# Performance work log

Measured on AMD Instinct MI355X. Metric: run time of the kernel, lower is better.

Reference implementation:

```python
import jax, jax.numpy as jnp
from jax import lax
import numpy as np

NDIM = 256
BATCH = 65536
NROT = NDIM * (NDIM - 1) // 2  # comb(ndim, 2) = 32640


def _givens_mat(rots, ii, jj, ndim):
    """Product G_last @ ... @ G_1 of Givens rotations in combinations order.

    Left-multiplying by G(i, j, theta) only modifies rows i and j, so we apply
    each rotation as a rank-2 row update instead of a full matmul (same math
    as the original `plane_rot_mat @ mat` loop).
    """
    def step(mat, carry):
        i, j, th = carry
        c = jnp.cos(th)
        s = jnp.sin(th)
        ri = mat[i]
        rj = mat[j]
        mat = mat.at[i].set(c * ri - s * rj)
        mat = mat.at[j].set(s * ri + c * rj)
        return mat, None

    mat0 = jnp.eye(ndim, dtype=jnp.complex64)
    mat, _ = lax.scan(step, mat0, (ii, jj, rots))
    return mat


def setup_inputs() -> dict:
    key = jax.random.key(0)
    k1, k2, k3, k4 = jax.random.split(key, 4)
    x = jax.random.normal(k1, (BATCH, NDIM), dtype=jnp.float32)
    rots1 = 0.1 * jax.random.normal(k2, (NROT,), dtype=jnp.float32)
    phases = 0.1 * jax.random.normal(k3, (NDIM,), dtype=jnp.float32)
    rots2 = 0.1 * jax.random.normal(k4, (NROT,), dtype=jnp.float32)
    return {"x": x, "rots1": rots1, "phases": phases, "rots2": rots2}


def reference(x, rots1, phases, rots2):
    ndim = x.shape[1]
    # np.triu_indices(ndim, 1) enumerates (i, j) pairs in the same row-major
    # order as itertools.combinations(range(ndim), 2).
    ii_np, jj_np = np.triu_indices(ndim, k=1)
    ii = jnp.asarray(ii_np, dtype=jnp.int32)
    jj = jnp.asarray(jj_np, dtype=jnp.int32)

    # vector_norm: row-wise L2 normalization
    xn = x / jnp.linalg.norm(x, axis=1, keepdims=True)
    xc = xn.astype(jnp.complex64)

    # rot1: y = x @ M1.T with M1 = G_last @ ... @ G_1
    M1 = _givens_mat(rots1, ii, jj, ndim)
    y = xc @ M1.T

    # phase_transforms: x @ diag(exp(i*phases)) == elementwise phase multiply
    y = y * jnp.exp(1j * phases)

    # rot2
    M2 = _givens_mat(rots2, ii, jj, ndim)
    y = y @ M2.T

    # measure: |.|^2
    return jnp.abs(y) ** 2
```

## Files before the change

kernel.cpp:

```cpp
#include <hip/hip_runtime.h>
#include <stdint.h>
#include <math.h>

#define NDIM 256
#define BATCH 65536
#define NROT 32640

typedef float  f32x4 __attribute__((ext_vector_type(4)));
typedef short  s16x8 __attribute__((ext_vector_type(8)));
typedef unsigned int u32x4 __attribute__((ext_vector_type(4)));
typedef unsigned int u32x2 __attribute__((ext_vector_type(2)));

static __device__ __forceinline__ unsigned short f2bf(float f) {
    unsigned int u = __float_as_uint(f);
    u += 0x7fffu + ((u >> 16) & 1u);
    return (unsigned short)(u >> 16);
}
static __device__ __forceinline__ float bf2f(unsigned short h) {
    return __uint_as_float(((unsigned)h) << 16);
}

static __device__ __forceinline__ void split4(f32x4 v, u32x2* hi, u32x2* lo) {
    unsigned short h[4], l[4];
    #pragma unroll
    for (int i = 0; i < 4; i++) {
        h[i] = f2bf(v[i]);
        l[i] = f2bf(v[i] - bf2f(h[i]));
    }
    *hi = (u32x2){ (unsigned)h[0] | ((unsigned)h[1] << 16),
                   (unsigned)h[2] | ((unsigned)h[3] << 16) };
    *lo = (u32x2){ (unsigned)l[0] | ((unsigned)l[1] << 16),
                   (unsigned)l[2] | ((unsigned)l[3] << 16) };
}
static __device__ __forceinline__ void split8(const float* v, u32x4* hi, u32x4* lo) {
    unsigned short h[8], l[8];
    #pragma unroll
    for (int i = 0; i < 8; i++) {
        h[i] = f2bf(v[i]);
        l[i] = f2bf(v[i] - bf2f(h[i]));
    }
    *hi = (u32x4){ (unsigned)h[0] | ((unsigned)h[1] << 16),
                   (unsigned)h[2] | ((unsigned)h[3] << 16),
                   (unsigned)h[4] | ((unsigned)h[5] << 16),
                   (unsigned)h[6] | ((unsigned)h[7] << 16) };
    *lo = (u32x4){ (unsigned)l[0] | ((unsigned)l[1] << 16),
                   (unsigned)l[2] | ((unsigned)l[3] << 16),
                   (unsigned)l[4] | ((unsigned)l[5] << 16),
                   (unsigned)l[6] | ((unsigned)l[7] << 16) };
}

static __device__ __forceinline__ int sweep_bound(int k, int pblk) {
    int target = k * (NROT / pblk);
    int best = 0, bd = 0x7fffffff;
    for (int i = 0; i <= 256; i += 4) {
        int pre = i * 255 - (i * (i - 1)) / 2;
        int d = pre - target; d = (d < 0) ? -d : d;
        if (d < bd) { bd = d; best = i; }
    }
    return best;
}

__global__ __launch_bounds__(64) void k_blocks(const float* __restrict__ r1,
                                               const float* __restrict__ r2,
                                               float* __restrict__ bmats, int pblk,
                                               const float* __restrict__ xg,
                                               unsigned short* __restrict__ xbf) {
    __shared__ float colb[264 * 64];
    __shared__ float2 csb[256 * 4];
    __shared__ float2 tri[24 * 6];
    const int nblk = 8 * pblk;

    if ((int)blockIdx.x >= nblk) {
        const int lane = threadIdx.x;
        const int r0 = ((int)blockIdx.x - nblk) * 16;
        #pragma unroll
        for (int hb = 0; hb < 2; hb++) {
            f32x4 v[8];
            #pragma unroll
            for (int i = 0; i < 8; i++)
                v[i] = *(const f32x4*)&xg[(size_t)(r0 + hb * 8 + i) * 256 + lane * 4];
            #pragma unroll
            for (int i = 0; i < 8; i++) {
                float s = v[i][0] * v[i][0] + v[i][1] * v[i][1]
                        + v[i][2] * v[i][2] + v[i][3] * v[i][3];
                #pragma unroll
                for (int off = 32; off; off >>= 1) s += __shfl_xor(s, off, 64);
                float sc = 1.0f / sqrtf(s);
                unsigned short h0 = f2bf(v[i][0] * sc), h1 = f2bf(v[i][1] * sc);
                unsigned short h2 = f2bf(v[i][2] * sc), h3 = f2bf(v[i][3] * sc);
                u32x2 pk = { (unsigned)h0 | ((unsigned)h1 << 16),
                             (unsigned)h2 | ((unsigned)h3 << 16) };
                *(u32x2*)&xbf[(size_t)(r0 + hb * 8 + i) * 256 + lane * 4] = pk;
            }
        }
        return;
    }

    const int t = threadIdx.x;
    const int bid = blockIdx.x;
    const int chunk = bid & 3;
    const int b = (bid >> 2) % pblk;
    const int set = (bid >> 2) / pblk;
    const int col0 = chunk * 64;
    const float* rots = set ? r2 : r1;

    const int s0 = sweep_bound(b, pblk);
    const int s1 = sweep_bound(b + 1, pblk);
    const int ngroups = (s1 - s0) >> 2;

    {
        const f32x4 z = {0.f, 0.f, 0.f, 0.f};
        #pragma unroll 11
        for (int q = 0; q < 66; q++)
            *(f32x4*)&colb[(q * 64 + t) * 4] = z;
        colb[(col0 + t) * 64 + t] = 1.0f;
    }

    for (int k = t; k < ngroups * 6; k += 64) {
        int g = k / 6, q = k - g * 6;
        int a  = (q < 3) ? 0 : ((q < 5) ? 1 : 2);
        int bb = (q < 3) ? (q + 1) : ((q < 5) ? (q - 1) : 3);
        int m0 = s0 + g * 4;
        int m = m0 + a;
        int base = m * 255 - (m * (m - 1)) / 2;
        float th = rots[base - m - 1 + (m0 + bb)];
        float sv, cv; sincosf(th, &sv, &cv);
        tri[k] = make_float2(cv, sv);
    }

    for (int g = 0; g < ngroups; g++) {
        const int m0 = s0 + g * 4;
        int off[4];
        #pragma unroll
        for (int a = 0; a < 4; a++) {
            int m = m0 + a;
            int base = m * 255 - (m * (m - 1)) / 2;
            off[a] = base - m - 1;
        }
        const int n_j = 252 - m0;
        const int n_p = (n_j > 0) ? ((n_j + 7) & ~7) : 0;

        for (int k = t; k < n_p * 4; k += 64) {
            int jj = k >> 2, a = k & 3;
            int j = m0 + 4 + jj;
            if (j < 256) {
                float th = rots[off[a] + j];
                float sv, cv; sincosf(th, &sv, &cv);
                csb[k] = make_float2(cv, sv);
            } else {
                csb[k] = make_float2(1.f, 0.f);
            }
        }

        float u0 = colb[(m0 + 0) * 64 + t];
        float u1 = colb[(m0 + 1) * 64 + t];
        float u2 = colb[(m0 + 2) * 64 + t];
        float u3 = colb[(m0 + 3) * 64 + t];

        {
            float2 cv; float nr;
            cv = tri[g * 6 + 0]; nr = cv.y * u0 + cv.x * u1; u0 = cv.x * u0 - cv.y * u1; u1 = nr;
            cv = tri[g * 6 + 1]; nr = cv.y * u0 + cv.x * u2; u0 = cv.x * u0 - cv.y * u2; u2 = nr;
            cv = tri[g * 6 + 2]; nr = cv.y * u0 + cv.x * u3; u0 = cv.x * u0 - cv.y * u3; u3 = nr;
            cv = tri[g * 6 + 3]; nr = cv.y * u1 + cv.x * u2; u1 = cv.x * u1 - cv.y * u2; u2 = nr;
            cv = tri[g * 6 + 4]; nr = cv.y * u1 + cv.x * u3; u1 = cv.x * u1 - cv.y * u3; u3 = nr;
            cv = tri[g * 6 + 5]; nr = cv.y * u2 + cv.x * u3; u2 = cv.x * u2 - cv.y * u3; u3 = nr;
        }

        if (n_p > 0) {
            float rbuf[8];
            #pragma unroll
            for (int p = 0; p < 8; p++)
                rbuf[p] = colb[(m0 + 4 + p) * 64 + t];
            for (int c = 0; c < n_p; c += 8) {
                #pragma unroll
                for (int p = 0; p < 8; p++) {
                    const int j = m0 + 4 + c + p;
                    float r = rbuf[p];
                    int jn = j + 8; jn = (jn < 263) ? jn : 263;
                    rbuf[p] = colb[jn * 64 + t];
                    float2 a0 = csb[(c + p) * 4 + 0];
                    float2 a1 = csb[(c + p) * 4 + 1];
                    float2 a2 = csb[(c + p) * 4 + 2];
                    float2 a3 = csb[(c + p) * 4 + 3];
                    float nr;
                    nr = a0.y * u0 + a0.x * r; u0 = a0.x * u0 - a0.y * r; r = nr;
                    nr = a1.y * u1 + a1.x * r; u1 = a1.x * u1 - a1.y * r; r = nr;
                    nr = a2.y * u2 + a2.x * r; u2 = a2.x * u2 - a2.y * r; r = nr;
                    nr = a3.y * u3 + a3.x * r; u3 = a3.x * u3 - a3.y * r; r = nr;
                    colb[j * 64 + t] = r;
                }
            }
        }
        colb[(m0 + 0) * 64 + t] = u0;
        colb[(m0 + 1) * 64 + t] = u1;
        colb[(m0 + 2) * 64 + t] = u2;
        colb[(m0 + 3) * 64 + t] = u3;
    }

    float* outm = bmats + (size_t)(set * pblk + b) * 65536;
    for (int r = 0; r < 256; r++)
        outm[(size_t)r * 256 + col0 + t] = colb[r * 64 + t];
}

__global__ __launch_bounds__(256) void k_combine(const float* __restrict__ src,
                                                 float* __restrict__ dst,
                                                 int half, int pblk) {
    const int by = blockIdx.y;
    const int set = by / half, pidx = by % half;
    const int stride = pblk / (2 * half);
    const int s0A = sweep_bound((2 * pidx + 1) * stride, pblk);
    const float* Am = src + (size_t)(set * 2 * half + 2 * pidx + 1) * 65536;
    const float* Bm = src + (size_t)(set * 2 * half + 2 * pidx) * 65536;
    float* Dm = dst + (size_t)(set * half + pidx) * 65536;
    const int tr = blockIdx.x >> 2, tc = blockIdx.x & 3;
    const int tid = threadIdx.x;

    if (tr * 64 + 64 <= s0A) {
        #pragma unroll
        for (int it = 0; it < 4; it++) {
            int flat = tid + it * 256;
            int r = flat >> 4, c4 = flat & 15;
            size_t idx = (size_t)(tr * 64 + r) * 256 + tc * 64 + c4 * 4;
            *(f32x4*)&Dm[idx] = *(const f32x4*)&Bm[idx];
        }
        return;
    }
    const int kb0 = (tr * 64 >= s0A) ? (s0A >> 5) : 0;

    __shared__ unsigned short Ahi[64 * 40], Alo[64 * 40];
    __shared__ unsigned short Bhi[64 * 40], Blo[64 * 40];

    const int lane = tid & 63, w = tid >> 6;
    const int mh = (w >> 1) * 32, nh = (w & 1) * 32;
    const int l15 = lane & 15, lq = lane >> 4;
    const int bn = tid & 63, bkq = tid >> 6;

    f32x4 acc[2][2];
    #pragma unroll
    for (int i = 0; i < 2; i++)
        #pragma unroll
        for (int j = 0; j < 2; j++) acc[i][j] = (f32x4){0.f, 0.f, 0.f, 0.f};

    for (int kb = kb0; kb < 8; kb++) {
        __syncthreads();
        #pragma unroll
        for (int it = 0; it < 2; it++) {
            int flat = tid + it * 256;
            int r = flat >> 3, c4 = flat & 7;
            f32x4 v = *(const f32x4*)&Am[(size_t)(tr * 64 + r) * 256 + kb * 32 + c4 * 4];
            u32x2 hi, lo; split4(v, &hi, &lo);
            *(u32x2*)&Ahi[r * 40 + c4 * 4] = hi;
            *(u32x2*)&Alo[r * 40 + c4 * 4] = lo;
        }
        {
            float bv[8];
            #pragma unroll
            for (int i = 0; i < 8; i++)
                bv[i] = Bm[(size_t)(kb * 32 + bkq * 8 + i) * 256 + tc * 64 + bn];
            u32x4 hi, lo; split8(bv, &hi, &lo);
            *(u32x4*)&Bhi[bn * 40 + bkq * 8] = hi;
            *(u32x4*)&Blo[bn * 40 + bkq * 8] = lo;
        }
        __syncthreads();
        s16x8 ah[2], al[2], bh[2], bl[2];
        #pragma unroll
        for (int tm = 0; tm < 2; tm++) {
            ah[tm] = *(const s16x8*)&Ahi[(mh + tm * 16 + l15) * 40 + lq * 8];
            al[tm] = *(const s16x8*)&Alo[(mh + tm * 16 + l15) * 40 + lq * 8];
        }
        #pragma unroll
        for (int tn = 0; tn < 2; tn++) {
            bh[tn] = *(const s16x8*)&Bhi[(nh + tn * 16 + l15) * 40 + lq * 8];
            bl[tn] = *(const s16x8*)&Blo[(nh + tn * 16 + l15) * 40 + lq * 8];
        }
        #pragma unroll
        for (int tm = 0; tm < 2; tm++)
            #pragma unroll
            for (int tn = 0; tn < 2; tn++) {
                acc[tm][tn] = __builtin_amdgcn_mfma_f32_16x16x32_bf16(ah[tm], bh[tn], acc[tm][tn], 0, 0, 0);
                acc[tm][tn] = __builtin_amdgcn_mfma_f32_16x16x32_bf16(ah[tm], bl[tn], acc[tm][tn], 0, 0, 0);
                acc[tm][tn] = __builtin_amdgcn_mfma_f32_16x16x32_bf16(al[tm], bh[tn], acc[tm][tn], 0, 0, 0);
            }
    }
    #pragma unroll
    for (int tm = 0; tm < 2; tm++)
        #pragma unroll
        for (int tn = 0; tn < 2; tn++)
            #pragma unroll
            for (int r = 0; r < 4; r++)
                Dm[(size_t)(tr * 64 + mh + tm * 16 + lq * 4 + r) * 256
                   + tc * 64 + nh + tn * 16 + l15] = acc[tm][tn][r];
}

__global__ __launch_bounds__(256) void k_abt(const float* __restrict__ mats,
                                             const float* __restrict__ phases,
                                             unsigned short* __restrict__ abt) {
    const float* Am = mats + 65536;
    const float* Bm = mats;
    const int v = blockIdx.y;
    const int tr = blockIdx.x >> 2, tc = blockIdx.x & 3;
    const int tid = threadIdx.x;

    __shared__ unsigned short Ahi[64 * 40], Alo[64 * 40];
    __shared__ unsigned short Bhi[64 * 40], Blo[64 * 40];

    const int lane = tid & 63, w = tid >> 6;
    const int mh = (w >> 1) * 32, nh = (w & 1) * 32;
    const int l15 = lane & 15, lq = lane >> 4;
    const int bn = tid & 63, bkq = tid >> 6;

    f32x4 acc[2][2];
    #pragma unroll
    for (int i = 0; i < 2; i++)
        #pragma unroll
        for (int j = 0; j < 2; j++) acc[i][j] = (f32x4){0.f, 0.f, 0.f, 0.f};

    for (int kb = 0; kb < 8; kb++) {
        __syncthreads();
        #pragma unroll
        for (int it = 0; it < 2; it++) {
            int flat = tid + it * 256;
            int r = flat >> 3, c4 = flat & 7;
            f32x4 vv = *(const f32x4*)&Am[(size_t)(tr * 64 + r) * 256 + kb * 32 + c4 * 4];
            u32x2 hi, lo; split4(vv, &hi, &lo);
            *(u32x2*)&Ahi[r * 40 + c4 * 4] = hi;
            *(u32x2*)&Alo[r * 40 + c4 * 4] = lo;
        }
        {
            float bv[8];
            #pragma unroll
            for (int i = 0; i < 8; i++) {
                int kg = kb * 32 + bkq * 8 + i;
                float ph = phases[kg];
                float sc = v ? sinf(ph) : cosf(ph);
                bv[i] = Bm[(size_t)kg * 256 + tc * 64 + bn] * sc;
            }
            u32x4 hi, lo; split8(bv, &hi, &lo);
            *(u32x4*)&Bhi[bn * 40 + bkq * 8] = hi;
            *(u32x4*)&Blo[bn * 40 + bkq * 8] = lo;
        }
        __syncthreads();
        s16x8 ah[2], al[2], bh[2], bl[2];
        #pragma unroll
        for (int tm = 0; tm < 2; tm++) {
            ah[tm] = *(const s16x8*)&Ahi[(mh + tm * 16 + l15) * 40 + lq * 8];
            al[tm] = *(const s16x8*)&Alo[(mh + tm * 16 + l15) * 40 + lq * 8];
        }
        #pragma unroll
        for (int tn = 0; tn < 2; tn++) {
            bh[tn] = *(const s16x8*)&Bhi[(nh + tn * 16 + l15) * 40 + lq * 8];
            bl[tn] = *(const s16x8*)&Blo[(nh + tn * 16 + l15) * 40 + lq * 8];
        }
        #pragma unroll
        for (int tm = 0; tm < 2; tm++)
            #pragma unroll
            for (int tn = 0; tn < 2; tn++) {
                acc[tm][tn] = __builtin_amdgcn_mfma_f32_16x16x32_bf16(ah[tm], bh[tn], acc[tm][tn], 0, 0, 0);
                acc[tm][tn] = __builtin_amdgcn_mfma_f32_16x16x32_bf16(ah[tm], bl[tn], acc[tm][tn], 0, 0, 0);
                acc[tm][tn] = __builtin_amdgcn_mfma_f32_16x16x32_bf16(al[tm], bh[tn], acc[tm][tn], 0, 0, 0);
            }
    }
    #pragma unroll
    for (int tm = 0; tm < 2; tm++)
        #pragma unroll
        for (int tn = 0; tn < 2; tn++)
            #pragma unroll
            for (int r = 0; r < 4; r++)
                abt[(size_t)(v * 256 + tr * 64 + mh + tm * 16 + lq * 4 + r) * 256
                    + tc * 64 + nh + tn * 16 + l15] = f2bf(acc[tm][tn][r]);
}

__global__ __launch_bounds__(256) void k_norm(const float* __restrict__ x,
                                              float* __restrict__ invn) {
    const int row = blockIdx.x * 4 + (threadIdx.x >> 6);
    const int lane = threadIdx.x & 63;
    f32x4 v = *(const f32x4*)&x[(size_t)row * 256 + lane * 4];
    float s = v[0] * v[0] + v[1] * v[1] + v[2] * v[2] + v[3] * v[3];
    for (int off = 32; off; off >>= 1) s += __shfl_xor(s, off, 64);
    if (lane == 0) invn[row] = 1.0f / sqrtf(s);
}

#define BKP 136
__global__ __launch_bounds__(256) void k_gemm_bf(const unsigned short* __restrict__ xbf,
                                                 const unsigned short* __restrict__ abt,
                                                 float* __restrict__ out) {
    __shared__ unsigned short As[128 * BKP];
    __shared__ unsigned short Bs[128 * BKP];
    const int tid = threadIdx.x;
    const int cb = blockIdx.x;
    const int rb = blockIdx.y;
    const int lane = tid & 63, w = tid >> 6;

    f32x4 acc[16];
    #pragma unroll
    for (int i = 0; i < 16; i++) acc[i] = (f32x4){0.f, 0.f, 0.f, 0.f};

    int rA[8], cA[8], grB[8];
    #pragma unroll
    for (int it = 0; it < 8; it++) {
        int flat = tid + it * 256;
        rA[it] = flat >> 4; cA[it] = flat & 15;
        int r = rA[it];
        grB[it] = (r < 64) ? (cb * 64 + r) : (256 + cb * 64 + (r - 64));
    }

    u32x4 pa[8], pb[8];
    #pragma unroll
    for (int it = 0; it < 8; it++) {
        pa[it] = *(const u32x4*)&xbf[(size_t)(rb * 128 + rA[it]) * 256 + cA[it] * 8];
        pb[it] = *(const u32x4*)&abt[(size_t)grB[it] * 256 + cA[it] * 8];
    }
    #pragma unroll
    for (int it = 0; it < 8; it++) {
        *(u32x4*)&As[rA[it] * BKP + cA[it] * 8] = pa[it];
        *(u32x4*)&Bs[rA[it] * BKP + cA[it] * 8] = pb[it];
    }
    __syncthreads();
    #pragma unroll
    for (int it = 0; it < 8; it++) {
        pa[it] = *(const u32x4*)&xbf[(size_t)(rb * 128 + rA[it]) * 256 + 128 + cA[it] * 8];
        pb[it] = *(const u32x4*)&abt[(size_t)grB[it] * 256 + 128 + cA[it] * 8];
    }

    auto compute = [&]() {
        #pragma unroll
        for (int ks = 0; ks < 4; ks++) {
            const int k0 = ks * 32 + (lane >> 4) * 8;
            s16x8 a[2], b[8];
            #pragma unroll
            for (int tm = 0; tm < 2; tm++)
                a[tm] = *(const s16x8*)&As[(w * 32 + tm * 16 + (lane & 15)) * BKP + k0];
            #pragma unroll
            for (int tn = 0; tn < 8; tn++)
                b[tn] = *(const s16x8*)&Bs[(tn * 16 + (lane & 15)) * BKP + k0];
            #pragma unroll
            for (int tm = 0; tm < 2; tm++)
                #pragma unroll
                for (int tn = 0; tn < 8; tn++)
                    acc[tm * 8 + tn] = __builtin_amdgcn_mfma_f32_16x16x32_bf16(
                        a[tm], b[tn], acc[tm * 8 + tn], 0, 0, 0);
        }
    };
    compute();
    __syncthreads();
    #pragma unroll
    for (int it = 0; it < 8; it++) {
        *(u32x4*)&As[rA[it] * BKP + cA[it] * 8] = pa[it];
        *(u32x4*)&Bs[rA[it] * BKP + cA[it] * 8] = pb[it];
    }
    __syncthreads();
    compute();

    const int qr = lane >> 4, c = lane & 15;
    #pragma unroll
    for (int tm = 0; tm < 2; tm++) {
        #pragma unroll
        for (int tn = 0; tn < 4; tn++) {
            f32x4 p = acc[tm * 8 + tn];
            f32x4 q = acc[tm * 8 + tn + 4];
            #pragma unroll
            for (int r = 0; r < 4; r++) {
                int m = w * 32 + tm * 16 + qr * 4 + r;
                out[(size_t)(rb * 128 + m) * 256 + cb * 64 + tn * 16 + c] =
                    p[r] * p[r] + q[r] * q[r];
            }
        }
    }
}

__global__ __launch_bounds__(256) void k_gemm_f32(const float* __restrict__ x,
                                                  const unsigned short* __restrict__ abt,
                                                  const float* __restrict__ invn,
                                                  float* __restrict__ out) {
    __shared__ unsigned short As[128 * BKP];
    __shared__ unsigned short Bs[128 * BKP];
    const int tid = threadIdx.x;
    const int cb = blockIdx.x;
    const int rb = blockIdx.y;
    const int lane = tid & 63, w = tid >> 6;

    f32x4 acc[16];
    #pragma unroll
    for (int i = 0; i < 16; i++) acc[i] = (f32x4){0.f, 0.f, 0.f, 0.f};

    for (int kb = 0; kb < 2; kb++) {
        __syncthreads();
        #pragma unroll
        for (int it = 0; it < 16; it++) {
            int flat = tid + it * 256;
            int r = flat >> 5, c4 = flat & 31;
            f32x4 v = *(const f32x4*)&x[(size_t)(rb * 128 + r) * 256 + kb * 128 + c4 * 4];
            float sc = invn[rb * 128 + r];
            v[0] *= sc; v[1] *= sc; v[2] *= sc; v[3] *= sc;
            unsigned short h0 = f2bf(v[0]), h1 = f2bf(v[1]);
            unsigned short h2 = f2bf(v[2]), h3 = f2bf(v[3]);
            u32x2 pk = { (unsigned)h0 | ((unsigned)h1 << 16),
                         (unsigned)h2 | ((unsigned)h3 << 16) };
            *(u32x2*)&As[r * BKP + c4 * 4] = pk;
        }
        #pragma unroll
        for (int it = 0; it < 8; it++) {
            int flat = tid + it * 256;
            int r = flat >> 4, c8 = flat & 15;
            int gr = (r < 64) ? (cb * 64 + r) : (256 + cb * 64 + (r - 64));
            u32x4 vv = *(const u32x4*)&abt[(size_t)gr * 256 + kb * 128 + c8 * 8];
            *(u32x4*)&Bs[r * BKP + c8 * 8] = vv;
        }
        __syncthreads();
        #pragma unroll
        for (int ks = 0; ks < 4; ks++) {
            const int k0 = ks * 32 + (lane >> 4) * 8;
            s16x8 a[2], b[8];
            #pragma unroll
            for (int tm = 0; tm < 2; tm++)
                a[tm] = *(const s16x8*)&As[(w * 32 + tm * 16 + (lane & 15)) * BKP + k0];
            #pragma unroll
            for (int tn = 0; tn < 8; tn++)
                b[tn] = *(const s16x8*)&Bs[(tn * 16 + (lane & 15)) * BKP + k0];
            #pragma unroll
            for (int tm = 0; tm < 2; tm++)
                #pragma unroll
                for (int tn = 0; tn < 8; tn++)
                    acc[tm * 8 + tn] = __builtin_amdgcn_mfma_f32_16x16x32_bf16(
                        a[tm], b[tn], acc[tm * 8 + tn], 0, 0, 0);
        }
    }

    const int qr = lane >> 4, c = lane & 15;
    #pragma unroll
    for (int tm = 0; tm < 2; tm++) {
        #pragma unroll
        for (int tn = 0; tn < 4; tn++) {
            f32x4 p = acc[tm * 8 + tn];
            f32x4 q = acc[tm * 8 + tn + 4];
            #pragma unroll
            for (int r = 0; r < 4; r++) {
                int m = w * 32 + tm * 16 + qr * 4 + r;
                out[(size_t)(rb * 128 + m) * 256 + cb * 64 + tn * 16 + c] =
                    p[r] * p[r] + q[r] * q[r];
            }
        }
    }
}

extern "C" void kernel_launch(void* const* d_in, const int* in_sizes, int n_in,
                              void* d_out, int out_size, void* d_ws, size_t ws_size,
                              hipStream_t stream) {
    (void)in_sizes; (void)n_in; (void)out_size;
    const float* x      = (const float*)d_in[0];
    const float* rots1  = (const float*)d_in[1];
    const float* phases = (const float*)d_in[2];
    const float* rots2  = (const float*)d_in[3];
    float* out = (float*)d_out;
    char* ws = (char*)d_ws;

    const size_t MAT = 262144;
    int pblk = 32;
    while (pblk > 16 &&
           (size_t)3 * pblk * MAT + 2 * MAT + (size_t)BATCH * 512 > ws_size)
        pblk >>= 1;
    const size_t offA   = 0;
    const size_t offB   = offA + (size_t)2 * pblk * MAT;
    const size_t offABT = offB + (size_t)pblk * MAT;
    const size_t offINV = offABT + MAT;
    const size_t offXBF = offINV + MAT;
    const bool use_xbf = (offXBF + (size_t)BATCH * 512) <= ws_size;

    float*          A    = (float*)(ws + offA);
    float*          B    = (float*)(ws + offB);
    unsigned short* abt  = (unsigned short*)(ws + offABT);
    float*          invn = (float*)(ws + offINV);
    unsigned short* xbf  = (unsigned short*)(ws + offXBF);

    const int nblk = 8 * pblk;
    const int nxn  = use_xbf ? (BATCH / 16) : 0;
    k_blocks<<<nblk + nxn, 64, 0, stream>>>(rots1, rots2, A, pblk, x, xbf);

    float* srcp = A; float* dstp = B;
    for (int half = pblk / 2; half >= 1; half >>= 1) {
        k_combine<<<dim3(16, 2 * half), 256, 0, stream>>>(srcp, dstp, half, pblk);
        float* tmp = srcp; srcp = dstp; dstp = tmp;
    }
    k_abt<<<dim3(16, 2), 256, 0, stream>>>(srcp, phases, abt);

    if (use_xbf) {
        k_gemm_bf<<<dim3(4, BATCH / 128), 256, 0, stream>>>(xbf, abt, out);
    } else {
        k_norm<<<BATCH / 4, 256, 0, stream>>>(x, invn);
        k_gemm_f32<<<dim3(4, BATCH / 128), 256, 0, stream>>>(x, abt, invn, out);
    }
}
```

Measured before the change: 269.7 us.

## Precompute Givens sincos in a separate kernel and move normalization into first combine

Adds a small kernel that computes cos/sin for all rotations once into workspace, so k_blocks reads precomputed pairs instead of calling sincosf per element. The row normalization and bf16 conversion of x moves out of k_blocks and into extra blocks of the first k_combine launch, using one wave per row with 64 rows per block. The intent is to shorten the serial block-building phase and overlap the memory-bound normalization with combine work. It adds one kernel launch and reuses the B buffer as sincos scratch before combine overwrites it.

```diff
diff --git a/kernel.cpp b/kernel.cpp
--- a/kernel.cpp
+++ b/kernel.cpp
@@ -60,41 +60,20 @@
     return best;
 }
 
-__global__ __launch_bounds__(64) void k_blocks(const float* __restrict__ r1,
-                                               const float* __restrict__ r2,
-                                               float* __restrict__ bmats, int pblk,
-                                               const float* __restrict__ xg,
-                                               unsigned short* __restrict__ xbf) {
+__global__ __launch_bounds__(256) void k_cs(const float* __restrict__ r1,
+                                            const float* __restrict__ r2,
+                                            float2* __restrict__ cs) {
+    int i = blockIdx.x * 256 + threadIdx.x;
+    float th = (i < NROT) ? r1[i] : r2[i - NROT];
+    float sv, cv; sincosf(th, &sv, &cv);
+    cs[i] = make_float2(cv, sv);
+}
+
+__global__ __launch_bounds__(64) void k_blocks(const float2* __restrict__ cs,
+                                               float* __restrict__ bmats, int pblk) {
     __shared__ float colb[264 * 64];
     __shared__ float2 csb[256 * 4];
     __shared__ float2 tri[24 * 6];
-    const int nblk = 8 * pblk;
-
-    if ((int)blockIdx.x >= nblk) {
-        const int lane = threadIdx.x;
-        const int r0 = ((int)blockIdx.x - nblk) * 16;
-        #pragma unroll
-        for (int hb = 0; hb < 2; hb++) {
-            f32x4 v[8];
-            #pragma unroll
-            for (int i = 0; i < 8; i++)
-                v[i] = *(const f32x4*)&xg[(size_t)(r0 + hb * 8 + i) * 256 + lane * 4];
-            #pragma unroll
-            for (int i = 0; i < 8; i++) {
-                float s = v[i][0] * v[i][0] + v[i][1] * v[i][1]
-                        + v[i][2] * v[i][2] + v[i][3] * v[i][3];
-                #pragma unroll
-                for (int off = 32; off; off >>= 1) s += __shfl_xor(s, off, 64);
-                float sc = 1.0f / sqrtf(s);
-                unsigned short h0 = f2bf(v[i][0] * sc), h1 = f2bf(v[i][1] * sc);
-                unsigned short h2 = f2bf(v[i][2] * sc), h3 = f2bf(v[i][3] * sc);
-                u32x2 pk = { (unsigned)h0 | ((unsigned)h1 << 16),
-                             (unsigned)h2 | ((unsigned)h3 << 16) };
-                *(u32x2*)&xbf[(size_t)(r0 + hb * 8 + i) * 256 + lane * 4] = pk;
-            }
-        }
-        return;
-    }
 
     const int t = threadIdx.x;
     const int bid = blockIdx.x;
@@ -102,7 +81,7 @@
     const int b = (bid >> 2) % pblk;
     const int set = (bid >> 2) / pblk;
     const int col0 = chunk * 64;
-    const float* rots = set ? r2 : r1;
+    const float2* cst = cs + (size_t)set * NROT;
 
     const int s0 = sweep_bound(b, pblk);
     const int s1 = sweep_bound(b + 1, pblk);
@@ -123,9 +102,7 @@
         int m0 = s0 + g * 4;
         int m = m0 + a;
         int base = m * 255 - (m * (m - 1)) / 2;
-        float th = rots[base - m - 1 + (m0 + bb)];
-        float sv, cv; sincosf(th, &sv, &cv);
-        tri[k] = make_float2(cv, sv);
+        tri[k] = cst[base - m - 1 + m0 + bb];
     }
 
     for (int g = 0; g < ngroups; g++) {
@@ -140,15 +117,16 @@
         const int n_j = 252 - m0;
         const int n_p = (n_j > 0) ? ((n_j + 7) & ~7) : 0;
 
-        for (int k = t; k < n_p * 4; k += 64) {
-            int jj = k >> 2, a = k & 3;
-            int j = m0 + 4 + jj;
-            if (j < 256) {
-                float th = rots[off[a] + j];
-                float sv, cv; sincosf(th, &sv, &cv);
-                csb[k] = make_float2(cv, sv);
-            } else {
-                csb[k] = make_float2(1.f, 0.f);
+        {
+            const int kmax = n_p * 4;
+            #pragma unroll 4
+            for (int it = 0; it < 16; it++) {
+                int k = t + it * 64;
+                if (k < kmax) {
+                    int jj = k >> 2, a = k & 3;
+                    int j = m0 + 4 + jj;
+                    csb[k] = (j < 256) ? cst[off[a] + j] : make_float2(1.f, 0.f);
+                }
             }
         }
 
@@ -205,8 +183,33 @@
 
 __global__ __launch_bounds__(256) void k_combine(const float* __restrict__ src,
                                                  float* __restrict__ dst,
-                                                 int half, int pblk) {
+                                                 int half, int pblk,
+                                                 const float* __restrict__ xg,
+                                                 unsigned short* __restrict__ xbf) {
     const int by = blockIdx.y;
+    const int tid = threadIdx.x;
+
+    if (by >= 2 * half) {
+        const int id = (by - 2 * half) * 16 + blockIdx.x;
+        const int w = tid >> 6, lane = tid & 63;
+        const int r0 = id * 64;
+        #pragma unroll 2
+        for (int p = 0; p < 16; p++) {
+            int row = r0 + p * 4 + w;
+            f32x4 v = *(const f32x4*)&xg[(size_t)row * 256 + lane * 4];
+            float s = v[0] * v[0] + v[1] * v[1] + v[2] * v[2] + v[3] * v[3];
+            #pragma unroll
+            for (int off = 32; off; off >>= 1) s += __shfl_xor(s, off, 64);
+            float sc = 1.0f / sqrtf(s);
+            unsigned short h0 = f2bf(v[0] * sc), h1 = f2bf(v[1] * sc);
+            unsigned short h2 = f2bf(v[2] * sc), h3 = f2bf(v[3] * sc);
+            u32x2 pk = { (unsigned)h0 | ((unsigned)h1 << 16),
+                         (unsigned)h2 | ((unsigned)h3 << 16) };
+            *(u32x2*)&xbf[(size_t)row * 256 + lane * 4] = pk;
+        }
+        return;
+    }
+
     const int set = by / half, pidx = by % half;
     const int stride = pblk / (2 * half);
     const int s0A = sweep_bound((2 * pidx + 1) * stride, pblk);
@@ -214,7 +217,6 @@
     const float* Bm = src + (size_t)(set * 2 * half + 2 * pidx) * 65536;
     float* Dm = dst + (size_t)(set * half + pidx) * 65536;
     const int tr = blockIdx.x >> 2, tc = blockIdx.x & 3;
-    const int tid = threadIdx.x;
 
     if (tr * 64 + 64 <= s0A) {
         #pragma unroll
@@ -572,15 +574,19 @@
     unsigned short* abt  = (unsigned short*)(ws + offABT);
     float*          invn = (float*)(ws + offINV);
     unsigned short* xbf  = (unsigned short*)(ws + offXBF);
-
-    const int nblk = 8 * pblk;
-    const int nxn  = use_xbf ? (BATCH / 16) : 0;
-    k_blocks<<<nblk + nxn, 64, 0, stream>>>(rots1, rots2, A, pblk, x, xbf);
+    float2*         cs   = (float2*)(ws + offB);
+
+    k_cs<<<(2 * NROT) / 256, 256, 0, stream>>>(rots1, rots2, cs);
+    k_blocks<<<8 * pblk, 64, 0, stream>>>(cs, A, pblk);
 
     float* srcp = A; float* dstp = B;
+    bool first = true;
     for (int half = pblk / 2; half >= 1; half >>= 1) {
-        k_combine<<<dim3(16, 2 * half), 256, 0, stream>>>(srcp, dstp, half, pblk);
+        const int xny = (first && use_xbf) ? 64 : 0;
+        k_combine<<<dim3(16, 2 * half + xny), 256, 0, stream>>>(srcp, dstp, half, pblk,
+                                                                x, xbf);
         float* tmp = srcp; srcp = dstp; dstp = tmp;
+        first = false;
     }
     k_abt<<<dim3(16, 2), 256, 0, stream>>>(srcp, phases, abt);
 
```

After: 274.2 us. No clear change (+1.7%).
